# Optimization experiments

Measured on AMD Instinct MI355X. Metric: run time of the kernel, lower is better.

The kernel has to match this reference:

```python
import jax, jax.numpy as jnp
import numpy as np

N = 50000          # nodes
E = 800000         # edges (avg degree 16)
H, D = 4, 32       # heads, per-head channels; hidden = H*D = 128
DIMS_IN = [32, 128, 128]


def setup_inputs() -> dict:
    key = jax.random.key(0)
    ks = jax.random.split(key, 40)
    inp = {}
    inp["x"] = jax.random.normal(ks[0], (N, 32), jnp.float32)
    inp["edge_index"] = jax.random.randint(ks[1], (2, E), 0, N, dtype=jnp.int32)
    i = 2
    for l, din in enumerate(DIMS_IN):
        for nm in ["q", "k", "v", "s"]:
            inp[f"W{nm}{l}"] = jax.random.normal(ks[i], (din, H * D), jnp.float32) / np.float32(np.sqrt(din)); i += 1
            inp[f"b{nm}{l}"] = jax.random.normal(ks[i], (H * D,), jnp.float32) * 0.01; i += 1
    inp["Wf"] = jax.random.normal(ks[i], (H * D, 1), jnp.float32) / np.float32(np.sqrt(H * D)); i += 1
    inp["bf"] = jax.random.normal(ks[i], (1,), jnp.float32) * 0.01
    return inp


def _transformer_conv(x, src, dst, Wq, bq, Wk, bk, Wv, bv, Ws, bs):
    """PyG TransformerConv (concat=True, root_weight=True, beta=False, eval mode)."""
    n = x.shape[0]
    q = (x @ Wq + bq).reshape(n, H, D)   # queries at nodes
    k = (x @ Wk + bk).reshape(n, H, D)
    v = (x @ Wv + bv).reshape(n, H, D)
    # per-edge attention score: q at destination, k at source
    s = jnp.einsum("ehd,ehd->eh", q[dst], k[src]) / np.float32(np.sqrt(D))  # [E,H]
    # segment softmax over incoming edges of each destination node
    m = jax.ops.segment_max(s, dst, num_segments=n)          # [N,H]
    e = jnp.exp(s - m[dst])                                  # [E,H]
    den = jax.ops.segment_sum(e, dst, num_segments=n)        # [N,H]
    alpha = e / den[dst]                                     # [E,H]
    agg = jax.ops.segment_sum(alpha[:, :, None] * v[src], dst, num_segments=n)  # [N,H,D]
    return agg.reshape(n, H * D) + (x @ Ws + bs)             # skip connection


def reference(x, edge_index,
              Wq0, bq0, Wk0, bk0, Wv0, bv0, Ws0, bs0,
              Wq1, bq1, Wk1, bk1, Wv1, bv1, Ws1, bs1,
              Wq2, bq2, Wk2, bk2, Wv2, bv2, Ws2, bs2,
              Wf, bf):
    src, dst = edge_index[0], edge_index[1]
    layers = [
        (Wq0, bq0, Wk0, bk0, Wv0, bv0, Ws0, bs0),
        (Wq1, bq1, Wk1, bk1, Wv1, bv1, Ws1, bs1),
        (Wq2, bq2, Wk2, bk2, Wv2, bv2, Ws2, bs2),
    ]
    h = x
    for p in layers:
        h = jax.nn.relu(_transformer_conv(h, src, dst, *p))
    out = jax.nn.sigmoid(h @ Wf + bf)  # [N,1]
    return out
```

## Files before the change

kernel.cpp:

```cpp
#include <hip/hip_runtime.h>
#include <hip/hip_bf16.h>
#include <cstdint>
#include <cstddef>

typedef __attribute__((ext_vector_type(8))) short bf16x8;
typedef __attribute__((ext_vector_type(4))) float f32x4;

__device__ __forceinline__ unsigned short f2bs(float f){
  __hip_bfloat16 h = __float2bfloat16(f);
  return *(unsigned short*)&h;
}
__device__ __forceinline__ float bflo(unsigned int u){ return __uint_as_float(u << 16); }
__device__ __forceinline__ float bfhi(unsigned int u){ return __uint_as_float(u & 0xffff0000u); }
__device__ __forceinline__ void unp8(uint4 u, float* f){
  f[0]=bflo(u.x); f[1]=bfhi(u.x); f[2]=bflo(u.y); f[3]=bfhi(u.y);
  f[4]=bflo(u.z); f[5]=bfhi(u.z); f[6]=bflo(u.w); f[7]=bfhi(u.w);
}

__global__ void zero_int_kernel(int* __restrict__ p, int n){
  int i = blockIdx.x*256 + threadIdx.x;
  if (i < n) p[i] = 0;
}

__global__ void hist_kernel(const int* __restrict__ dst, int E, int* __restrict__ deg){
  int e = blockIdx.x*256 + threadIdx.x;
  if (e < E) atomicAdd(&deg[dst[e]], 1);
}

__global__ __launch_bounds__(1024)
void scanA_kernel(const int* __restrict__ deg, int n, int* __restrict__ rowptr, int* __restrict__ bsums){
  __shared__ int s[1024];
  int t = threadIdx.x;
  int i = blockIdx.x*1024 + t;
  int v = (i < n) ? deg[i] : 0;
  s[t] = v;
  __syncthreads();
  #pragma unroll
  for (int off = 1; off < 1024; off <<= 1){
    int a = (t >= off) ? s[t-off] : 0;
    __syncthreads();
    s[t] += a;
    __syncthreads();
  }
  if (i < n) rowptr[i] = s[t] - v;
  if (t == 1023) bsums[blockIdx.x] = s[1023];
}

__global__ void scanB_kernel(const int* __restrict__ bsums, int nch, int* __restrict__ choff){
  int t = threadIdx.x;
  int v = (t < nch) ? bsums[t] : 0;
  int x = v;
  #pragma unroll
  for (int off = 1; off < 64; off <<= 1){
    int u = __shfl_up(x, off, 64);
    if (t >= off) x += u;
  }
  choff[t] = x - v;
}

__global__ __launch_bounds__(1024)
void scanC_kernel(const int* __restrict__ choff, int n, int* __restrict__ rowptr, int* __restrict__ cursor){
  int i = blockIdx.x*1024 + threadIdx.x;
  if (i < n){
    int r = rowptr[i] + choff[blockIdx.x];
    rowptr[i] = r;
    cursor[i] = r;
  }
}

__global__ void scatter_kernel(const int* __restrict__ src, const int* __restrict__ dst, int E,
                               int* __restrict__ cursor, int* __restrict__ adj){
  int e = blockIdx.x*256 + threadIdx.x;
  if (e < E){
    int pos = atomicAdd(&cursor[dst[e]], 1);
    adj[pos] = src[e];
  }
}

struct PrepArgs {
  const float* w[12];
  unsigned short* o[12];
};

__global__ void transpose_w_kernel(PrepArgs a){
  int m = blockIdx.y;
  int K = (m < 4) ? 32 : 128;
  int halfK = K >> 1;
  int tot = 128 * halfK;
  int e = blockIdx.x*256 + threadIdx.x;
  if (e >= tot) return;
  int n  = e / halfK;
  int k2 = e % halfK;
  const float* W = a.w[m];
  unsigned int lo = __float_as_uint(W[(2*k2)  *128 + n]) >> 16;
  unsigned int hi = __float_as_uint(W[(2*k2+1)*128 + n]) & 0xffff0000u;
  ((unsigned int*)a.o[m])[e] = lo | hi;
}

__global__ void cvt_x_kernel(const float* __restrict__ x, unsigned short* __restrict__ xb, int n2){
  int i = blockIdx.x*256 + threadIdx.x;
  if (i < n2){
    float2 v = ((const float2*)x)[i];
    ((unsigned int*)xb)[i] = (__float_as_uint(v.x) >> 16) | (__float_as_uint(v.y) & 0xffff0000u);
  }
}

template<int DIN>
__global__ __launch_bounds__(256)
void gemm4_mfma(const unsigned short* __restrict__ X, int nn,
                const unsigned short* __restrict__ T0, const unsigned short* __restrict__ T1,
                const unsigned short* __restrict__ T2, const unsigned short* __restrict__ T3,
                const float* __restrict__ b0, const float* __restrict__ b1,
                const float* __restrict__ b2, const float* __restrict__ b3,
                unsigned short* __restrict__ O0, unsigned short* __restrict__ O1,
                unsigned short* __restrict__ O2, unsigned short* __restrict__ O3)
{
  constexpr int KP = DIN + 8;
  __shared__ __align__(16) unsigned short wt[128*KP];
  int t = threadIdx.x;
  int msel = blockIdx.y;
  const unsigned short* WT = (msel==0)?T0:(msel==1)?T1:(msel==2)?T2:T3;
  const float* B = (msel==0)?b0:(msel==1)?b1:(msel==2)?b2:b3;
  unsigned short* O = (msel==0)?O0:(msel==1)?O1:(msel==2)?O2:O3;

  {
    const int NU = 128*DIN/8;
    for (int u = t; u < NU; u += 256){
      uint4 v = ((const uint4*)WT)[u];
      int n = u / (DIN/8), b = u % (DIN/8);
      *(uint4*)&wt[n*KP + b*8] = v;
    }
  }

  int lane = t & 63, wv = t >> 6;
  int m0 = blockIdx.x*64 + wv*16;
  int n16 = lane & 15, quad = lane >> 4;

  bf16x8 af[DIN/32];
  {
    const unsigned short* xrow = X + (size_t)(m0 + n16)*DIN + quad*8;
    #pragma unroll
    for (int s = 0; s < DIN/32; s++) af[s] = *(const bf16x8*)(xrow + s*32);
  }

  __syncthreads();

  f32x4 acc[8];
  #pragma unroll
  for (int c=0;c<8;c++) acc[c] = (f32x4){0.f,0.f,0.f,0.f};

  #pragma unroll
  for (int s = 0; s < DIN/32; s++){
    #pragma unroll
    for (int c = 0; c < 8; c++){
      bf16x8 bf = *(const bf16x8*)&wt[(c*16 + n16)*KP + s*32 + quad*8];
      acc[c] = __builtin_amdgcn_mfma_f32_16x16x32_bf16(af[s], bf, acc[c], 0, 0, 0);
    }
  }

  #pragma unroll
  for (int c = 0; c < 8; c++){
    int col = c*16 + n16;
    float bias = B[col];
    #pragma unroll
    for (int r = 0; r < 4; r++){
      int row = m0 + quad*4 + r;
      if (row < nn) O[(size_t)row*128 + col] = f2bs(acc[c][r] + bias);
    }
  }
}

template<bool FINAL>
__global__ __launch_bounds__(256)
void attn_kernel(const unsigned short* __restrict__ q,  const unsigned short* __restrict__ kmat,
                 const unsigned short* __restrict__ vmat, const unsigned short* __restrict__ skip,
                 const int* __restrict__ rowptr, const int* __restrict__ deg,
                 const int* __restrict__ adj, unsigned short* __restrict__ hout,
                 const float* __restrict__ Wf, const float* __restrict__ bfp,
                 float* __restrict__ out, int nn)
{
  int lane = threadIdx.x & 63, wid = threadIdx.x >> 6;
  int n = blockIdx.x*4 + wid;
  if (n >= nn) return;
  int p = lane & 15, g = lane >> 4;
  const float RS = 0.17677669529663687f;

  float qf[8];
  { uint4 qu = *(const uint4*)(q + (size_t)n*128 + p*8); unp8(qu, qf); }

  int start = rowptr[n], dg = deg[n];
  float m = -INFINITY, l = 0.f;
  float acc[8];
  #pragma unroll
  for (int i=0;i<8;i++) acc[i]=0.f;

  for (int c0 = 0; c0 < dg; c0 += 64){
    int cn = min(64, dg - c0);
    int idx = adj[start + c0 + min(lane, cn-1)];
    int nit = (cn + 3) >> 2;

    bool val = g < cn;
    int s0 = __shfl(idx, min(g, cn-1), 64);
    uint4 ku = *(const uint4*)(kmat + (size_t)s0*128 + p*8);
    uint4 vu = *(const uint4*)(vmat + (size_t)s0*128 + p*8);

    for (int it = 0; it < nit; ++it){
      int j2 = (it+1)*4 + g;
      bool val2 = j2 < cn;
      int s2 = __shfl(idx, min(j2, cn-1), 64);
      uint4 ku2 = {0,0,0,0}, vu2 = {0,0,0,0};
      if (it + 1 < nit){
        ku2 = *(const uint4*)(kmat + (size_t)s2*128 + p*8);
        vu2 = *(const uint4*)(vmat + (size_t)s2*128 + p*8);
      }
      float kf[8]; unp8(ku, kf);
      float d = qf[0]*kf[0];
      #pragma unroll
      for (int i=1;i<8;i++) d = fmaf(qf[i], kf[i], d);
      d += __shfl_xor(d, 1, 64);
      d += __shfl_xor(d, 2, 64);
      float f = val ? d*RS : -INFINITY;
      float nm = fmaxf(m, f);
      float r = __expf(fmaxf(m - nm, -80.f));
      float w = __expf(fmaxf(f - nm, -80.f));
      m = nm;
      l = l*r + w;
      float vf[8]; unp8(vu, vf);
      #pragma unroll
      for (int i=0;i<8;i++) acc[i] = fmaf(w, vf[i], acc[i]*r);
      ku = ku2; vu = vu2; val = val2;
    }
  }

  float m1 = fmaxf(m, __shfl_xor(m, 16, 64));
  float M  = fmaxf(m1, __shfl_xor(m1, 32, 64));
  float sc = __expf(fmaxf(m - M, -80.f));
  float lp = l * sc;
  float l1 = lp + __shfl_xor(lp, 16, 64);
  float L  = l1 + __shfl_xor(l1, 32, 64);
  #pragma unroll
  for (int i=0;i<8;i++){
    float a = acc[i]*sc;
    a += __shfl_xor(a, 16, 64);
    a += __shfl_xor(a, 32, 64);
    acc[i] = a;
  }
  float inv = (L > 0.f) ? 1.f/L : 0.f;
  float sk[8];
  { uint4 su = *(const uint4*)(skip + (size_t)n*128 + p*8); unp8(su, sk); }
  float o[8];
  #pragma unroll
  for (int i=0;i<8;i++) o[i] = fmaxf(fmaf(acc[i], inv, sk[i]), 0.f);

  if constexpr (!FINAL){
    if (g == 0){
      uint4 st;
      st.x = (unsigned)f2bs(o[0]) | ((unsigned)f2bs(o[1])<<16);
      st.y = (unsigned)f2bs(o[2]) | ((unsigned)f2bs(o[3])<<16);
      st.z = (unsigned)f2bs(o[4]) | ((unsigned)f2bs(o[5])<<16);
      st.w = (unsigned)f2bs(o[6]) | ((unsigned)f2bs(o[7])<<16);
      *(uint4*)(hout + (size_t)n*128 + p*8) = st;
    }
  } else {
    float4 w0 = *(const float4*)(Wf + p*8);
    float4 w1 = *(const float4*)(Wf + p*8 + 4);
    float pd = o[0]*w0.x;
    pd = fmaf(o[1], w0.y, pd); pd = fmaf(o[2], w0.z, pd); pd = fmaf(o[3], w0.w, pd);
    pd = fmaf(o[4], w1.x, pd); pd = fmaf(o[5], w1.y, pd);
    pd = fmaf(o[6], w1.z, pd); pd = fmaf(o[7], w1.w, pd);
    pd += __shfl_xor(pd, 1, 64);
    pd += __shfl_xor(pd, 2, 64);
    pd += __shfl_xor(pd, 4, 64);
    pd += __shfl_xor(pd, 8, 64);
    if (lane == 0){
      float z = pd + bfp[0];
      out[n] = 1.f / (1.f + __expf(-z));
    }
  }
}

extern "C" void kernel_launch(void* const* d_in, const int* in_sizes, int n_in,
                              void* d_out, int out_size, void* d_ws, size_t ws_size,
                              hipStream_t stream) {
  const int N = in_sizes[0] / 32;
  const int E = in_sizes[1] / 2;
  const float* x = (const float*)d_in[0];
  const int* ei  = (const int*)d_in[1];
  const int* src = ei;
  const int* dst = ei + E;
  auto Wp = [&](int i){ return (const float*)d_in[i]; };
  const int NP = N + 64;

  char* p = (char*)d_ws;
  auto alloc = [&](size_t b){ char* r = p; p += (b + 255) & ~(size_t)255; return (void*)r; };
  unsigned short* F0 = (unsigned short*)alloc((size_t)NP*128*2);
  unsigned short* F1 = (unsigned short*)alloc((size_t)NP*128*2);
  unsigned short* Qb = (unsigned short*)alloc((size_t)NP*128*2);
  unsigned short* Kb = (unsigned short*)alloc((size_t)NP*128*2);
  unsigned short* Vb = (unsigned short*)alloc((size_t)NP*128*2);
  unsigned short* xb = (unsigned short*)alloc((size_t)NP*32*2);
  unsigned short* WT[12];
  for (int i = 0; i < 12; i++){
    int K = (i < 4) ? 32 : 128;
    WT[i] = (unsigned short*)alloc((size_t)128*K*2);
  }
  int* deg    = (int*)alloc((size_t)N*4);
  int* rowptr = (int*)alloc((size_t)N*4);
  int* cursor = (int*)alloc((size_t)N*4);
  int* adj    = (int*)alloc((size_t)E*4);
  int* bsums  = (int*)alloc(64*4);
  int* choff  = (int*)alloc(64*4);

  zero_int_kernel<<<(N+255)/256, 256, 0, stream>>>(deg, N);
  hist_kernel<<<(E+255)/256, 256, 0, stream>>>(dst, E, deg);
  int nch = (N + 1023) / 1024;
  scanA_kernel<<<nch, 1024, 0, stream>>>(deg, N, rowptr, bsums);
  scanB_kernel<<<1, 64, 0, stream>>>(bsums, nch, choff);
  scanC_kernel<<<nch, 1024, 0, stream>>>(choff, N, rowptr, cursor);
  scatter_kernel<<<(E+255)/256, 256, 0, stream>>>(src, dst, E, cursor, adj);

  PrepArgs pa;
  const int widx[12] = {2,4,6,8, 10,12,14,16, 18,20,22,24};
  for (int i = 0; i < 12; i++){ pa.w[i] = Wp(widx[i]); pa.o[i] = WT[i]; }
  transpose_w_kernel<<<dim3(32,12), 256, 0, stream>>>(pa);
  cvt_x_kernel<<<(N*16+255)/256, 256, 0, stream>>>(x, xb, N*16);

  dim3 gg((N+63)/64, 4);
  int ab = (N + 3) / 4;
  gemm4_mfma<32><<<gg, 256, 0, stream>>>(xb, N,
      WT[0],WT[1],WT[2],WT[3], Wp(3),Wp(5),Wp(7),Wp(9), Qb,Kb,Vb, F0);
  attn_kernel<false><<<ab, 256, 0, stream>>>(Qb,Kb,Vb, F0, rowptr,deg,adj, F0,
      nullptr, nullptr, nullptr, N);
  gemm4_mfma<128><<<gg, 256, 0, stream>>>(F0, N,
      WT[4],WT[5],WT[6],WT[7], Wp(11),Wp(13),Wp(15),Wp(17), Qb,Kb,Vb, F1);
  attn_kernel<false><<<ab, 256, 0, stream>>>(Qb,Kb,Vb, F1, rowptr,deg,adj, F1,
      nullptr, nullptr, nullptr, N);
  gemm4_mfma<128><<<gg, 256, 0, stream>>>(F1, N,
      WT[8],WT[9],WT[10],WT[11], Wp(19),Wp(21),Wp(23),Wp(25), Qb,Kb,Vb, F0);
  attn_kernel<true><<<ab, 256, 0, stream>>>(Qb,Kb,Vb, F0, rowptr,deg,adj, nullptr,
      Wp(26), Wp(27), (float*)d_out, N);
}
```

Measured before the change: 472.7 us.

## Process two edges per attention iteration with packed math, fuse prep and scan kernels

The attention loop now handles two neighbor edges per lane group per iteration, using packed float2 FMAs and issuing four gathers ahead instead of two. This is meant to raise memory-level parallelism and halve the number of online-softmax rescale steps. Separately, scanB is folded into scanC through a per-block reduction of bsums, the weight transpose and x conversion are merged into one kernel, and the zeroing kernel is replaced by hipMemsetAsync. Together these cut launch count, at the cost of more registers per thread and a grid-stride conversion spread over only 32 blocks.

```diff
diff --git a/kernel.cpp b/kernel.cpp
--- a/kernel.cpp
+++ b/kernel.cpp
@@ -5,6 +5,7 @@
 
 typedef __attribute__((ext_vector_type(8))) short bf16x8;
 typedef __attribute__((ext_vector_type(4))) float f32x4;
+typedef __attribute__((ext_vector_type(2))) float f32x2;
 
 __device__ __forceinline__ unsigned short f2bs(float f){
   __hip_bfloat16 h = __float2bfloat16(f);
@@ -12,14 +13,8 @@
 }
 __device__ __forceinline__ float bflo(unsigned int u){ return __uint_as_float(u << 16); }
 __device__ __forceinline__ float bfhi(unsigned int u){ return __uint_as_float(u & 0xffff0000u); }
-__device__ __forceinline__ void unp8(uint4 u, float* f){
-  f[0]=bflo(u.x); f[1]=bfhi(u.x); f[2]=bflo(u.y); f[3]=bfhi(u.y);
-  f[4]=bflo(u.z); f[5]=bfhi(u.z); f[6]=bflo(u.w); f[7]=bfhi(u.w);
-}
-
-__global__ void zero_int_kernel(int* __restrict__ p, int n){
-  int i = blockIdx.x*256 + threadIdx.x;
-  if (i < n) p[i] = 0;
+__device__ __forceinline__ f32x2 b2f2(unsigned int u){
+  return (f32x2){ __uint_as_float(u << 16), __uint_as_float(u & 0xffff0000u) };
 }
 
 __global__ void hist_kernel(const int* __restrict__ dst, int E, int* __restrict__ deg){
@@ -46,23 +41,21 @@
   if (t == 1023) bsums[blockIdx.x] = s[1023];
 }
 
-__global__ void scanB_kernel(const int* __restrict__ bsums, int nch, int* __restrict__ choff){
+__global__ __launch_bounds__(1024)
+void scanC_kernel(const int* __restrict__ bsums, int nch, int n,
+                  int* __restrict__ rowptr, int* __restrict__ cursor){
+  __shared__ int choff_s;
   int t = threadIdx.x;
-  int v = (t < nch) ? bsums[t] : 0;
-  int x = v;
-  #pragma unroll
-  for (int off = 1; off < 64; off <<= 1){
-    int u = __shfl_up(x, off, 64);
-    if (t >= off) x += u;
-  }
-  choff[t] = x - v;
-}
-
-__global__ __launch_bounds__(1024)
-void scanC_kernel(const int* __restrict__ choff, int n, int* __restrict__ rowptr, int* __restrict__ cursor){
-  int i = blockIdx.x*1024 + threadIdx.x;
+  if (t < 64){
+    int v = (t < nch && t < (int)blockIdx.x) ? bsums[t] : 0;
+    #pragma unroll
+    for (int off = 1; off <= 32; off <<= 1) v += __shfl_xor(v, off, 64);
+    if (t == 0) choff_s = v;
+  }
+  __syncthreads();
+  int i = blockIdx.x*1024 + t;
   if (i < n){
-    int r = rowptr[i] + choff[blockIdx.x];
+    int r = rowptr[i] + choff_s;
     rowptr[i] = r;
     cursor[i] = r;
   }
@@ -80,28 +73,30 @@
 struct PrepArgs {
   const float* w[12];
   unsigned short* o[12];
+  const float* x;
+  unsigned short* xb;
+  int n2;
 };
 
-__global__ void transpose_w_kernel(PrepArgs a){
+__global__ void prep_kernel(PrepArgs a){
   int m = blockIdx.y;
-  int K = (m < 4) ? 32 : 128;
-  int halfK = K >> 1;
-  int tot = 128 * halfK;
-  int e = blockIdx.x*256 + threadIdx.x;
-  if (e >= tot) return;
-  int n  = e / halfK;
-  int k2 = e % halfK;
-  const float* W = a.w[m];
-  unsigned int lo = __float_as_uint(W[(2*k2)  *128 + n]) >> 16;
-  unsigned int hi = __float_as_uint(W[(2*k2+1)*128 + n]) & 0xffff0000u;
-  ((unsigned int*)a.o[m])[e] = lo | hi;
-}
-
-__global__ void cvt_x_kernel(const float* __restrict__ x, unsigned short* __restrict__ xb, int n2){
-  int i = blockIdx.x*256 + threadIdx.x;
-  if (i < n2){
-    float2 v = ((const float2*)x)[i];
-    ((unsigned int*)xb)[i] = (__float_as_uint(v.x) >> 16) | (__float_as_uint(v.y) & 0xffff0000u);
+  if (m < 12){
+    int K = (m < 4) ? 32 : 128;
+    int halfK = K >> 1;
+    int tot = 128 * halfK;
+    int e = blockIdx.x*256 + threadIdx.x;
+    if (e >= tot) return;
+    int n  = e / halfK;
+    int k2 = e % halfK;
+    const float* W = a.w[m];
+    unsigned int lo = __float_as_uint(W[(2*k2)  *128 + n]) >> 16;
+    unsigned int hi = __float_as_uint(W[(2*k2+1)*128 + n]) & 0xffff0000u;
+    ((unsigned int*)a.o[m])[e] = lo | hi;
+  } else {
+    for (int i = blockIdx.x*256 + threadIdx.x; i < a.n2; i += 32*256){
+      float2 v = ((const float2*)a.x)[i];
+      ((unsigned int*)a.xb)[i] = (__float_as_uint(v.x) >> 16) | (__float_as_uint(v.y) & 0xffff0000u);
+    }
   }
 }
 
@@ -185,50 +180,72 @@
   int p = lane & 15, g = lane >> 4;
   const float RS = 0.17677669529663687f;
 
-  float qf[8];
-  { uint4 qu = *(const uint4*)(q + (size_t)n*128 + p*8); unp8(qu, qf); }
+  f32x2 qv[4];
+  { uint4 qu = *(const uint4*)(q + (size_t)n*128 + p*8);
+    qv[0]=b2f2(qu.x); qv[1]=b2f2(qu.y); qv[2]=b2f2(qu.z); qv[3]=b2f2(qu.w); }
 
   int start = rowptr[n], dg = deg[n];
   float m = -INFINITY, l = 0.f;
-  float acc[8];
-  #pragma unroll
-  for (int i=0;i<8;i++) acc[i]=0.f;
+  f32x2 acc[4] = {{0.f,0.f},{0.f,0.f},{0.f,0.f},{0.f,0.f}};
 
   for (int c0 = 0; c0 < dg; c0 += 64){
     int cn = min(64, dg - c0);
     int idx = adj[start + c0 + min(lane, cn-1)];
-    int nit = (cn + 3) >> 2;
-
-    bool val = g < cn;
-    int s0 = __shfl(idx, min(g, cn-1), 64);
-    uint4 ku = *(const uint4*)(kmat + (size_t)s0*128 + p*8);
-    uint4 vu = *(const uint4*)(vmat + (size_t)s0*128 + p*8);
+    int nit = (cn + 7) >> 3;
+
+    bool a0 = 2*g < cn, a1 = 2*g + 1 < cn;
+    int s0 = __shfl(idx, min(2*g    , cn-1), 64);
+    int s1 = __shfl(idx, min(2*g + 1, cn-1), 64);
+    uint4 ku0 = *(const uint4*)(kmat + (size_t)s0*128 + p*8);
+    uint4 ku1 = *(const uint4*)(kmat + (size_t)s1*128 + p*8);
+    uint4 vu0 = *(const uint4*)(vmat + (size_t)s0*128 + p*8);
+    uint4 vu1 = *(const uint4*)(vmat + (size_t)s1*128 + p*8);
 
     for (int it = 0; it < nit; ++it){
-      int j2 = (it+1)*4 + g;
-      bool val2 = j2 < cn;
-      int s2 = __shfl(idx, min(j2, cn-1), 64);
-      uint4 ku2 = {0,0,0,0}, vu2 = {0,0,0,0};
+      int jn0 = (it+1)*8 + 2*g;
+      bool b0 = jn0 < cn, b1 = jn0 + 1 < cn;
+      int t0 = __shfl(idx, min(jn0    , cn-1), 64);
+      int t1 = __shfl(idx, min(jn0 + 1, cn-1), 64);
+      uint4 kn0={0,0,0,0}, kn1={0,0,0,0}, vn0={0,0,0,0}, vn1={0,0,0,0};
       if (it + 1 < nit){
-        ku2 = *(const uint4*)(kmat + (size_t)s2*128 + p*8);
-        vu2 = *(const uint4*)(vmat + (size_t)s2*128 + p*8);
+        kn0 = *(const uint4*)(kmat + (size_t)t0*128 + p*8);
+        kn1 = *(const uint4*)(kmat + (size_t)t1*128 + p*8);
+        vn0 = *(const uint4*)(vmat + (size_t)t0*128 + p*8);
+        vn1 = *(const uint4*)(vmat + (size_t)t1*128 + p*8);
       }
-      float kf[8]; unp8(ku, kf);
-      float d = qf[0]*kf[0];
-      #pragma unroll
-      for (int i=1;i<8;i++) d = fmaf(qf[i], kf[i], d);
-      d += __shfl_xor(d, 1, 64);
-      d += __shfl_xor(d, 2, 64);
-      float f = val ? d*RS : -INFINITY;
-      float nm = fmaxf(m, f);
-      float r = __expf(fmaxf(m - nm, -80.f));
-      float w = __expf(fmaxf(f - nm, -80.f));
+      f32x2 d0v = qv[0]*b2f2(ku0.x);
+      d0v = __builtin_elementwise_fma(qv[1], b2f2(ku0.y), d0v);
+      d0v = __builtin_elementwise_fma(qv[2], b2f2(ku0.z), d0v);
+      d0v = __builtin_elementwise_fma(qv[3], b2f2(ku0.w), d0v);
+      f32x2 d1v = qv[0]*b2f2(ku1.x);
+      d1v = __builtin_elementwise_fma(qv[1], b2f2(ku1.y), d1v);
+      d1v = __builtin_elementwise_fma(qv[2], b2f2(ku1.z), d1v);
+      d1v = __builtin_elementwise_fma(qv[3], b2f2(ku1.w), d1v);
+      float d0 = d0v.x + d0v.y;
+      float d1 = d1v.x + d1v.y;
+      d0 += __shfl_xor(d0, 1, 64); d0 += __shfl_xor(d0, 2, 64);
+      d1 += __shfl_xor(d1, 1, 64); d1 += __shfl_xor(d1, 2, 64);
+      float f0 = a0 ? d0*RS : -INFINITY;
+      float f1 = a1 ? d1*RS : -INFINITY;
+
+      float nm = fmaxf(m, fmaxf(f0, f1));
+      float r  = __expf(fmaxf(m  - nm, -80.f));
+      float w0 = __expf(fmaxf(f0 - nm, -80.f));
+      float w1 = __expf(fmaxf(f1 - nm, -80.f));
       m = nm;
-      l = l*r + w;
-      float vf[8]; unp8(vu, vf);
-      #pragma unroll
-      for (int i=0;i<8;i++) acc[i] = fmaf(w, vf[i], acc[i]*r);
-      ku = ku2; vu = vu2; val = val2;
+      l = l*r + (w0 + w1);
+      f32x2 rr  = {r , r };
+      f32x2 w0v = {w0, w0};
+      f32x2 w1v = {w1, w1};
+      acc[0] = __builtin_elementwise_fma(w1v, b2f2(vu1.x),
+               __builtin_elementwise_fma(w0v, b2f2(vu0.x), acc[0]*rr));
+      acc[1] = __builtin_elementwise_fma(w1v, b2f2(vu1.y),
+               __builtin_elementwise_fma(w0v, b2f2(vu0.y), acc[1]*rr));
+      acc[2] = __builtin_elementwise_fma(w1v, b2f2(vu1.z),
+               __builtin_elementwise_fma(w0v, b2f2(vu0.z), acc[2]*rr));
+      acc[3] = __builtin_elementwise_fma(w1v, b2f2(vu1.w),
+               __builtin_elementwise_fma(w0v, b2f2(vu0.w), acc[3]*rr));
+      ku0=kn0; ku1=kn1; vu0=vn0; vu1=vn1; a0=b0; a1=b1;
     }
   }
 
@@ -236,21 +253,24 @@
   float M  = fmaxf(m1, __shfl_xor(m1, 32, 64));
   float sc = __expf(fmaxf(m - M, -80.f));
   float lp = l * sc;
-  float l1 = lp + __shfl_xor(lp, 16, 64);
-  float L  = l1 + __shfl_xor(l1, 32, 64);
-  #pragma unroll
-  for (int i=0;i<8;i++){
-    float a = acc[i]*sc;
-    a += __shfl_xor(a, 16, 64);
-    a += __shfl_xor(a, 32, 64);
-    acc[i] = a;
+  lp += __shfl_xor(lp, 16, 64);
+  float L = lp + __shfl_xor(lp, 32, 64);
+  f32x2 scv = {sc, sc};
+  float o[8];
+  #pragma unroll
+  for (int i=0;i<4;i++){
+    f32x2 a = acc[i]*scv;
+    a.x += __shfl_xor(a.x, 16, 64); a.y += __shfl_xor(a.y, 16, 64);
+    a.x += __shfl_xor(a.x, 32, 64); a.y += __shfl_xor(a.y, 32, 64);
+    o[2*i] = a.x; o[2*i+1] = a.y;
   }
   float inv = (L > 0.f) ? 1.f/L : 0.f;
   float sk[8];
-  { uint4 su = *(const uint4*)(skip + (size_t)n*128 + p*8); unp8(su, sk); }
-  float o[8];
-  #pragma unroll
-  for (int i=0;i<8;i++) o[i] = fmaxf(fmaf(acc[i], inv, sk[i]), 0.f);
+  { uint4 su = *(const uint4*)(skip + (size_t)n*128 + p*8);
+    sk[0]=bflo(su.x); sk[1]=bfhi(su.x); sk[2]=bflo(su.y); sk[3]=bfhi(su.y);
+    sk[4]=bflo(su.z); sk[5]=bfhi(su.z); sk[6]=bflo(su.w); sk[7]=bfhi(su.w); }
+  #pragma unroll
+  for (int i=0;i<8;i++) o[i] = fmaxf(fmaf(o[i], inv, sk[i]), 0.f);
 
   if constexpr (!FINAL){
     if (g == 0){
@@ -309,21 +329,19 @@
   int* cursor = (int*)alloc((size_t)N*4);
   int* adj    = (int*)alloc((size_t)E*4);
   int* bsums  = (int*)alloc(64*4);
-  int* choff  = (int*)alloc(64*4);
-
-  zero_int_kernel<<<(N+255)/256, 256, 0, stream>>>(deg, N);
+
+  hipMemsetAsync(deg, 0, (size_t)N*4, stream);
   hist_kernel<<<(E+255)/256, 256, 0, stream>>>(dst, E, deg);
   int nch = (N + 1023) / 1024;
   scanA_kernel<<<nch, 1024, 0, stream>>>(deg, N, rowptr, bsums);
-  scanB_kernel<<<1, 64, 0, stream>>>(bsums, nch, choff);
-  scanC_kernel<<<nch, 1024, 0, stream>>>(choff, N, rowptr, cursor);
+  scanC_kernel<<<nch, 1024, 0, stream>>>(bsums, nch, N, rowptr, cursor);
   scatter_kernel<<<(E+255)/256, 256, 0, stream>>>(src, dst, E, cursor, adj);
 
   PrepArgs pa;
   const int widx[12] = {2,4,6,8, 10,12,14,16, 18,20,22,24};
   for (int i = 0; i < 12; i++){ pa.w[i] = Wp(widx[i]); pa.o[i] = WT[i]; }
-  transpose_w_kernel<<<dim3(32,12), 256, 0, stream>>>(pa);
-  cvt_x_kernel<<<(N*16+255)/256, 256, 0, stream>>>(x, xb, N*16);
+  pa.x = x; pa.xb = xb; pa.n2 = N*16;
+  prep_kernel<<<dim3(32,13), 256, 0, stream>>>(pa);
 
   dim3 gg((N+63)/64, 4);
   int ab = (N + 3) / 4;
```

Measured after the change: 485.5 us. +2.7%, slower.
